# Kernel optimization log

Measured on AMD Instinct MI355X. Metric: run time of the kernel, lower is better.

## Reference

```python
import jax, jax.numpy as jnp
import numpy as np

T, H, F, E, K = 1024, 1024, 2048, 8, 2  # tokens, hidden, ffn_inter, experts, top_k


def setup_inputs() -> dict:
    key = jax.random.key(0)
    ks = jax.random.split(key, 7)
    return {
        "hidden_states": jax.random.normal(ks[0], (T, H), dtype=jnp.float32),
        "token_selected_experts": jax.random.randint(ks[1], (T, K), 0, E, dtype=jnp.int32),
        "token_final_scales": jax.random.uniform(ks[2], (T, K), dtype=jnp.float32),
        "w1": jax.random.normal(ks[3], (E, 2 * F, H), dtype=jnp.float32) * 0.02,  # gated fc1: [gate; linear]
        "b1": jax.random.normal(ks[4], (E, 2 * F), dtype=jnp.float32) * 0.02,
        "w2": jax.random.normal(ks[5], (E, H, F), dtype=jnp.float32) * 0.02,
        "b2": jax.random.normal(ks[6], (E, H), dtype=jnp.float32) * 0.02,
    }


def reference(hidden_states, token_selected_experts, token_final_scales, w1, b1, w2, b2):
    # Grouped GEMM fc1 over all experts: [T, E, 2F]
    h1 = jnp.einsum('th,efh->tef', hidden_states, w1) + b1[None]
    ffn = w2.shape[2]
    gate, lin = h1[..., :ffn], h1[..., ffn:]
    act = jax.nn.silu(gate) * lin                      # swiglu gated activation, [T, E, F]
    y_all = jnp.einsum('tef,ehf->teh', act, w2) + b2[None]  # fc2, [T, E, H]
    # Gather the top-k selected experts per token and combine with final scales
    sel = token_selected_experts.astype(jnp.int32)     # [T, K]
    y_sel = jnp.take_along_axis(y_all, sel[:, :, None], axis=1)  # [T, K, H]
    out = jnp.sum(y_sel * token_final_scales[:, :, None], axis=1)  # [T, H]
    return out
```

## Files before the change

kernel.cpp:

```cpp
#include <hip/hip_runtime.h>
#include <hip/hip_bf16.h>
#include <cstdint>
#include <cstddef>

#define TDIM 1024
#define HDIM 1024
#define FDIM 2048
#define NEXP 8
#define NENT 2048

typedef __bf16 bf16_t;
typedef __bf16 bf16x4 __attribute__((ext_vector_type(4)));
typedef __bf16 bf16x8 __attribute__((ext_vector_type(8)));
typedef float  f32x4  __attribute__((ext_vector_type(4)));

#define H_ELEMS ((size_t)TDIM*HDIM)

#define WB_OFFSETS 0
#define WB_ETOK    64
#define WB_ESCALE  (WB_ETOK + NENT*4)
#define WB_ACT     16512
#define WB_H       (WB_ACT + (size_t)NENT*FDIM*2)

__device__ __forceinline__ void gload16(const void* g, void* l) {
  __builtin_amdgcn_global_load_lds((const __attribute__((address_space(1))) void*)g,
                                   (__attribute__((address_space(3))) void*)l, 16, 0, 0);
}

__device__ __forceinline__ bf16x8 cvt8(const float4 a, const float4 b) {
  bf16x8 o;
  o[0]=(bf16_t)a.x; o[1]=(bf16_t)a.y; o[2]=(bf16_t)a.z; o[3]=(bf16_t)a.w;
  o[4]=(bf16_t)b.x; o[5]=(bf16_t)b.y; o[6]=(bf16_t)b.z; o[7]=(bf16_t)b.w;
  return o;
}

__device__ __forceinline__ int segswz(int seg, int row) {
  return seg ^ (row & 3) ^ ((row >> 2) & 3);
}

__global__ void route_all(const int* __restrict__ sel, const float* __restrict__ scal,
                          int* __restrict__ offsets, int* __restrict__ etok,
                          float* __restrict__ escale) {
  __shared__ int cnt[NEXP], cnt2[NEXP], offs[NEXP+1];
  const int t = threadIdx.x;
  if (t < NEXP) { cnt[t] = 0; cnt2[t] = 0; }
  __syncthreads();
  int e8[8];
  #pragma unroll
  for (int q = 0; q < 8; q++) {
    int i = t*8 + q;
    e8[q] = sel[i];
    atomicAdd(&cnt[e8[q]], 1);
  }
  __syncthreads();
  if (t == 0) {
    int s = 0;
    for (int e = 0; e < NEXP; e++) { offs[e] = s; offsets[e] = s; s += cnt[e]; }
    offs[NEXP] = s; offsets[NEXP] = s;
  }
  __syncthreads();
  #pragma unroll
  for (int q = 0; q < 8; q++) {
    int i = t*8 + q;
    int e = e8[q];
    int pos = offs[e] + atomicAdd(&cnt2[e], 1);
    etok[pos]   = i >> 1;
    escale[pos] = scal[i];
  }
}

__global__ void convert_h(const float* __restrict__ h, bf16_t* __restrict__ hbf) {
  size_t idx = ((size_t)blockIdx.x*256 + threadIdx.x) * 8;
  float4 v0 = ((const float4*)(h + idx))[0];
  float4 v1 = ((const float4*)(h + idx))[1];
  *(bf16x8*)(hbf + idx) = cvt8(v0, v1);
}


__global__ __launch_bounds__(256, 3) void gemm1_v8(
    const bf16_t* __restrict__ hbf, const float* __restrict__ w1,
    const float* __restrict__ b1, const int* __restrict__ offsets,
    const int* __restrict__ etok, bf16_t* __restrict__ act)
{
  const int e   = blockIdx.y;
  const int off = offsets[e];
  const int nt  = offsets[e+1] - off;
  const int m0  = blockIdx.z * 128;
  if (m0 >= nt) return;
  const int n0  = blockIdx.x * 64;

  __shared__ __align__(16) bf16_t As[2][128*32];
  __shared__ __align__(16) bf16_t Bg[2][64*32];
  __shared__ __align__(16) bf16_t Bl[2][64*32];

  const int tid  = threadIdx.x;
  const int w    = tid >> 6, lane = tid & 63;
  const int quad = lane >> 4, lr = lane & 15;
  const int wm   = w >> 1,  wn = w & 1;

  const bf16_t* asrc0; const bf16_t* asrc1;
  int arow0, arow1;
  {
    const int r0 = 0*64 + w*16 + (lane >> 2);
    const int r1 = 1*64 + w*16 + (lane >> 2);
    const int s0 = segswz(lane & 3, r0);
    const int s1 = segswz(lane & 3, r1);
    int e0 = m0 + r0; if (e0 > nt-1) e0 = nt-1;
    int e1 = m0 + r1; if (e1 > nt-1) e1 = nt-1;
    asrc0 = hbf + (size_t)etok[off + e0]*HDIM + s0*8;
    asrc1 = hbf + (size_t)etok[off + e1]*HDIM + s1*8;
    arow0 = (0*64 + w*16)*32;
    arow1 = (1*64 + w*16)*32;
  }

  const int br = tid >> 2, bs = tid & 3;
  const float* gsrc = w1 + ((size_t)e*2*FDIM + (size_t)(n0 + br))*HDIM + bs*8;
  const float* lsrc = gsrc + (size_t)FDIM*HDIM;
  const int bofs = br*32 + (segswz(bs, br) << 3);

  int aoff[4], boff[2];
  #pragma unroll
  for (int i = 0; i < 4; i++) {
    const int r = wm*64 + i*16 + lr;
    aoff[i] = r*32 + (segswz(quad, r) << 3);
  }
  #pragma unroll
  for (int j = 0; j < 2; j++) {
    const int r = wn*32 + j*16 + lr;
    boff[j] = r*32 + (segswz(quad, r) << 3);
  }

  f32x4 accg[4][2] = {}, accl[4][2] = {};
  float4 g4[2][2], l4[2][2];

#define G1_LOADB(SET, K0)                                                     \
  { const float4* p_ = (const float4*)(gsrc + (K0));                          \
    g4[SET][0]=p_[0]; g4[SET][1]=p_[1];                                       \
    const float4* q_ = (const float4*)(lsrc + (K0));                          \
    l4[SET][0]=q_[0]; l4[SET][1]=q_[1]; }

#define G1_WRITEB(NXT, SET)                                                   \
  { *(bf16x8*)&Bg[NXT][bofs] = cvt8(g4[SET][0], g4[SET][1]);                  \
    *(bf16x8*)&Bl[NXT][bofs] = cvt8(l4[SET][0], l4[SET][1]); }

#define G1_MFMA(CUR)                                                          \
  { bf16x8 af[4], gf[2], lf[2];                                               \
    _Pragma("unroll")                                                         \
    for (int i = 0; i < 4; i++) af[i] = *(const bf16x8*)&As[CUR][aoff[i]];    \
    _Pragma("unroll")                                                         \
    for (int j = 0; j < 2; j++) {                                             \
      gf[j] = *(const bf16x8*)&Bg[CUR][boff[j]];                              \
      lf[j] = *(const bf16x8*)&Bl[CUR][boff[j]];                              \
    }                                                                         \
    _Pragma("unroll")                                                         \
    for (int i = 0; i < 4; i++)                                               \
      _Pragma("unroll")                                                       \
      for (int j = 0; j < 2; j++) {                                           \
        accg[i][j] = __builtin_amdgcn_mfma_f32_16x16x32_bf16(af[i], gf[j], accg[i][j], 0, 0, 0); \
        accl[i][j] = __builtin_amdgcn_mfma_f32_16x16x32_bf16(af[i], lf[j], accl[i][j], 0, 0, 0); \
      } }

  G1_LOADB(0, 0);
  __builtin_amdgcn_sched_barrier(0);
  gload16(asrc0 + 0, &As[0][arow0]);
  gload16(asrc1 + 0, &As[0][arow1]);
  __builtin_amdgcn_sched_barrier(0);
  G1_WRITEB(0, 0);
  G1_LOADB(0, 32);
  G1_LOADB(1, 64);
  asm volatile("s_waitcnt vmcnt(8) lgkmcnt(0)" ::: "memory");
  __builtin_amdgcn_sched_barrier(0);
  __builtin_amdgcn_s_barrier();
  __builtin_amdgcn_sched_barrier(0);

#define G1_STEP(CUR, SET)                                                     \
  { G1_WRITEB((CUR)^1, SET);                                                  \
    __builtin_amdgcn_sched_barrier(0);                                        \
    gload16(asrc0 + k0 + 32, &As[(CUR)^1][arow0]);                            \
    gload16(asrc1 + k0 + 32, &As[(CUR)^1][arow1]);                            \
    __builtin_amdgcn_sched_barrier(0);                                        \
    G1_LOADB(SET, k0 + 96);                                                   \
    __builtin_amdgcn_sched_barrier(0);                                        \
    G1_MFMA(CUR);                                                             \
    asm volatile("s_waitcnt vmcnt(4) lgkmcnt(0)" ::: "memory");               \
    __builtin_amdgcn_sched_barrier(0);                                        \
    __builtin_amdgcn_s_barrier();                                             \
    __builtin_amdgcn_sched_barrier(0);                                        \
    k0 += 32; }

  int k0 = 0;
  while (k0 < 896) {
    G1_STEP(0, 0);
    G1_STEP(1, 1);
  }
  G1_STEP(0, 0);
  G1_WRITEB(0, 1);
  __builtin_amdgcn_sched_barrier(0);
  gload16(asrc0 + 960, &As[0][arow0]);
  gload16(asrc1 + 960, &As[0][arow1]);
  __builtin_amdgcn_sched_barrier(0);
  G1_MFMA(1);
  asm volatile("s_waitcnt vmcnt(0) lgkmcnt(0)" ::: "memory");
  __builtin_amdgcn_sched_barrier(0);
  __builtin_amdgcn_s_barrier();
  __builtin_amdgcn_sched_barrier(0);
  G1_WRITEB(1, 0);
  __builtin_amdgcn_sched_barrier(0);
  gload16(asrc0 + 992, &As[1][arow0]);
  gload16(asrc1 + 992, &As[1][arow1]);
  __builtin_amdgcn_sched_barrier(0);
  G1_MFMA(0);
  asm volatile("s_waitcnt vmcnt(0) lgkmcnt(0)" ::: "memory");
  __builtin_amdgcn_sched_barrier(0);
  __builtin_amdgcn_s_barrier();
  __builtin_amdgcn_sched_barrier(0);
  G1_MFMA(1);

#undef G1_STEP
#undef G1_MFMA
#undef G1_WRITEB
#undef G1_LOADB

  #pragma unroll
  for (int j = 0; j < 2; j++) {
    const int f = n0 + wn*32 + j*16 + lr;
    const float bg_ = b1[e*2*FDIM + f];
    const float bl_ = b1[e*2*FDIM + FDIM + f];
    #pragma unroll
    for (int i = 0; i < 4; i++) {
      #pragma unroll
      for (int r = 0; r < 4; r++) {
        const int m = wm*64 + i*16 + quad*4 + r;
        if (m0 + m < nt) {
          const float g = accg[i][j][r] + bg_;
          const float l = accl[i][j][r] + bl_;
          const float s = g / (1.f + __expf(-g)) * l;
          act[(size_t)(off + m0 + m)*FDIM + f] = (bf16_t)s;
        }
      }
    }
  }
}

__global__ __launch_bounds__(256, 3) void gemm2_v8(
    const bf16_t* __restrict__ act, const float* __restrict__ w2,
    const float* __restrict__ b2, const int* __restrict__ offsets,
    const int* __restrict__ etok, const float* __restrict__ escale,
    float* __restrict__ out)
{
  const int e   = blockIdx.y;
  const int off = offsets[e];
  const int nt  = offsets[e+1] - off;
  const int m0  = blockIdx.z * 128;
  if (m0 >= nt) return;
  const int n0  = (blockIdx.x >> 2) * 128;
  const int kc  = blockIdx.x & 3;
  const int kbeg = kc * (FDIM/4);

  __shared__ __align__(16) bf16_t As[2][128*32];
  __shared__ __align__(16) bf16_t Bs[2][128*32];

  const int tid  = threadIdx.x;
  const int w    = tid >> 6, lane = tid & 63;
  const int quad = lane >> 4, lr = lane & 15;
  const int wm   = w >> 1,  wn = w & 1;

  const bf16_t* asrc0; const bf16_t* asrc1;
  int arow0, arow1;
  {
    const int r0 = 0*64 + w*16 + (lane >> 2);
    const int r1 = 1*64 + w*16 + (lane >> 2);
    const int s0 = segswz(lane & 3, r0);
    const int s1 = segswz(lane & 3, r1);
    int e0 = m0 + r0; if (e0 > nt-1) e0 = nt-1;
    int e1 = m0 + r1; if (e1 > nt-1) e1 = nt-1;
    asrc0 = act + (size_t)(off + e0)*FDIM + kbeg + s0*8;
    asrc1 = act + (size_t)(off + e1)*FDIM + kbeg + s1*8;
    arow0 = (0*64 + w*16)*32;
    arow1 = (1*64 + w*16)*32;
  }

  const int br = tid >> 1, bc = tid & 1;
  const float* bsrc = w2 + ((size_t)e*HDIM + (size_t)(n0 + br))*FDIM + kbeg + bc*16;
  const int bofs0 = br*32 + (segswz(2*bc,   br) << 3);
  const int bofs1 = br*32 + (segswz(2*bc+1, br) << 3);

  int aoff[4], boff[4];
  #pragma unroll
  for (int i = 0; i < 4; i++) {
    const int r = wm*64 + i*16 + lr;
    aoff[i] = r*32 + (segswz(quad, r) << 3);
  }
  #pragma unroll
  for (int j = 0; j < 4; j++) {
    const int r = wn*64 + j*16 + lr;
    boff[j] = r*32 + (segswz(quad, r) << 3);
  }

  f32x4 acc[4][4] = {};
  float4 b4[2][4];

#define G2_LOADB(SET, K0)                                                     \
  { const float4* p_ = (const float4*)(bsrc + (K0));                          \
    b4[SET][0]=p_[0]; b4[SET][1]=p_[1]; b4[SET][2]=p_[2]; b4[SET][3]=p_[3]; }

#define G2_WRITEB(NXT, SET)                                                   \
  { *(bf16x8*)&Bs[NXT][bofs0] = cvt8(b4[SET][0], b4[SET][1]);                 \
    *(bf16x8*)&Bs[NXT][bofs1] = cvt8(b4[SET][2], b4[SET][3]); }

#define G2_MFMA(CUR)                                                          \
  { bf16x8 af[4], bfr[4];                                                     \
    _Pragma("unroll")                                                         \
    for (int i = 0; i < 4; i++) af[i] = *(const bf16x8*)&As[CUR][aoff[i]];    \
    _Pragma("unroll")                                                         \
    for (int j = 0; j < 4; j++) bfr[j] = *(const bf16x8*)&Bs[CUR][boff[j]];   \
    _Pragma("unroll")                                                         \
    for (int i = 0; i < 4; i++)                                               \
      _Pragma("unroll")                                                       \
      for (int j = 0; j < 4; j++)                                             \
        acc[i][j] = __builtin_amdgcn_mfma_f32_16x16x32_bf16(af[i], bfr[j], acc[i][j], 0, 0, 0); }

  G2_LOADB(0, 0);
  __builtin_amdgcn_sched_barrier(0);
  gload16(asrc0 + 0, &As[0][arow0]);
  gload16(asrc1 + 0, &As[0][arow1]);
  __builtin_amdgcn_sched_barrier(0);
  G2_WRITEB(0, 0);
  G2_LOADB(0, 32);
  G2_LOADB(1, 64);
  asm volatile("s_waitcnt vmcnt(8) lgkmcnt(0)" ::: "memory");
  __builtin_amdgcn_sched_barrier(0);
  __builtin_amdgcn_s_barrier();
  __builtin_amdgcn_sched_barrier(0);

#define G2_STEP(CUR, SET)                                                     \
  { G2_WRITEB((CUR)^1, SET);                                                  \
    __builtin_amdgcn_sched_barrier(0);                                        \
    gload16(asrc0 + k0 + 32, &As[(CUR)^1][arow0]);                            \
    gload16(asrc1 + k0 + 32, &As[(CUR)^1][arow1]);                            \
    __builtin_amdgcn_sched_barrier(0);                                        \
    G2_LOADB(SET, k0 + 96);                                                   \
    __builtin_amdgcn_sched_barrier(0);                                        \
    G2_MFMA(CUR);                                                             \
    asm volatile("s_waitcnt vmcnt(4) lgkmcnt(0)" ::: "memory");               \
    __builtin_amdgcn_sched_barrier(0);                                        \
    __builtin_amdgcn_s_barrier();                                             \
    __builtin_amdgcn_sched_barrier(0);                                        \
    k0 += 32; }

  int k0 = 0;
  while (k0 < 384) {
    G2_STEP(0, 0);
    G2_STEP(1, 1);
  }
  G2_STEP(0, 0);
  G2_WRITEB(0, 1);
  __builtin_amdgcn_sched_barrier(0);
  gload16(asrc0 + 448, &As[0][arow0]);
  gload16(asrc1 + 448, &As[0][arow1]);
  __builtin_amdgcn_sched_barrier(0);
  G2_MFMA(1);
  asm volatile("s_waitcnt vmcnt(0) lgkmcnt(0)" ::: "memory");
  __builtin_amdgcn_sched_barrier(0);
  __builtin_amdgcn_s_barrier();
  __builtin_amdgcn_sched_barrier(0);
  G2_WRITEB(1, 0);
  __builtin_amdgcn_sched_barrier(0);
  gload16(asrc0 + 480, &As[1][arow0]);
  gload16(asrc1 + 480, &As[1][arow1]);
  __builtin_amdgcn_sched_barrier(0);
  G2_MFMA(0);
  asm volatile("s_waitcnt vmcnt(0) lgkmcnt(0)" ::: "memory");
  __builtin_amdgcn_sched_barrier(0);
  __builtin_amdgcn_s_barrier();
  __builtin_amdgcn_sched_barrier(0);
  G2_MFMA(1);

#undef G2_STEP
#undef G2_MFMA
#undef G2_WRITEB
#undef G2_LOADB

  #pragma unroll
  for (int i = 0; i < 4; i++) {
    #pragma unroll
    for (int r = 0; r < 4; r++) {
      const int m = wm*64 + i*16 + quad*4 + r;
      if (m0 + m < nt) {
        const int slot = off + m0 + m;
        const int t    = etok[slot];
        const float s  = escale[slot];
        #pragma unroll
        for (int j = 0; j < 4; j++) {
          const int n = n0 + wn*64 + j*16 + lr;
          float v = acc[i][j][r];
          if (kc == 0) v += b2[e*HDIM + n];
          atomicAdd(&out[(size_t)t*HDIM + n], s * v);
        }
      }
    }
  }
}

extern "C" void kernel_launch(void* const* d_in, const int* in_sizes, int n_in,
                              void* d_out, int out_size, void* d_ws, size_t ws_size,
                              hipStream_t stream) {
  const float* hidden = (const float*)d_in[0];
  const int*   sel    = (const int*)d_in[1];
  const float* scal   = (const float*)d_in[2];
  const float* w1     = (const float*)d_in[3];
  const float* b1     = (const float*)d_in[4];
  const float* w2     = (const float*)d_in[5];
  const float* b2     = (const float*)d_in[6];
  float* out = (float*)d_out;

  char* ws = (char*)d_ws;
  int*    offsets = (int*)(ws + WB_OFFSETS);
  int*    etok    = (int*)(ws + WB_ETOK);
  float*  escale  = (float*)(ws + WB_ESCALE);
  bf16_t* act     = (bf16_t*)(ws + WB_ACT);
  bf16_t* hbf     = (bf16_t*)(ws + WB_H);

  hipMemsetAsync(d_out, 0, (size_t)out_size * sizeof(float), stream);

  route_all<<<1, 256, 0, stream>>>(sel, scal, offsets, etok, escale);
  convert_h<<<(int)(H_ELEMS/8/256), 256, 0, stream>>>(hidden, hbf);

  gemm1_v8<<<dim3(FDIM/64, NEXP, NENT/128), 256, 0, stream>>>(hbf, w1, b1, offsets, etok, act);
  gemm2_v8<<<dim3((HDIM/128)*4, NEXP, NENT/128), 256, 0, stream>>>(act, w2, b2, offsets, etok, escale, out);
}
```

Before: 328.5 us.

## Double M tile to 256 rows with 512-thread blocks in both expert GEMMs

Both grouped GEMM kernels now use 512-thread blocks covering 256 token rows instead of 128, so each fp32 weight tile is loaded and converted to bf16 once for twice as many tokens. Weight-loading work per thread halves and the vmcnt wait counts are adjusted to match. In exchange, fewer blocks are launched, the last M tile of each expert is padded to 256 rows, and launch bounds now allow only one block per CU. Each expert holds about 256 routed rows on average, so some experts may still need a second, mostly empty tile.

```diff
diff --git a/kernel.cpp b/kernel.cpp
--- a/kernel.cpp
+++ b/kernel.cpp
@@ -77,7 +77,7 @@
 }
 
 
-__global__ __launch_bounds__(256, 3) void gemm1_v8(
+__global__ __launch_bounds__(512, 1) void gemm1_v9(
     const bf16_t* __restrict__ hbf, const float* __restrict__ w1,
     const float* __restrict__ b1, const int* __restrict__ offsets,
     const int* __restrict__ etok, bf16_t* __restrict__ act)
@@ -85,13 +85,12 @@
   const int e   = blockIdx.y;
   const int off = offsets[e];
   const int nt  = offsets[e+1] - off;
-  const int m0  = blockIdx.z * 128;
+  const int m0  = blockIdx.z * 256;
   if (m0 >= nt) return;
   const int n0  = blockIdx.x * 64;
 
-  __shared__ __align__(16) bf16_t As[2][128*32];
-  __shared__ __align__(16) bf16_t Bg[2][64*32];
-  __shared__ __align__(16) bf16_t Bl[2][64*32];
+  __shared__ __align__(16) bf16_t As[2][256*32];
+  __shared__ __align__(16) bf16_t Bs[2][2*64*32];
 
   const int tid  = threadIdx.x;
   const int w    = tid >> 6, lane = tid & 63;
@@ -101,22 +100,22 @@
   const bf16_t* asrc0; const bf16_t* asrc1;
   int arow0, arow1;
   {
-    const int r0 = 0*64 + w*16 + (lane >> 2);
-    const int r1 = 1*64 + w*16 + (lane >> 2);
+    const int r0 = 0*128 + w*16 + (lane >> 2);
+    const int r1 = 1*128 + w*16 + (lane >> 2);
     const int s0 = segswz(lane & 3, r0);
     const int s1 = segswz(lane & 3, r1);
     int e0 = m0 + r0; if (e0 > nt-1) e0 = nt-1;
     int e1 = m0 + r1; if (e1 > nt-1) e1 = nt-1;
     asrc0 = hbf + (size_t)etok[off + e0]*HDIM + s0*8;
     asrc1 = hbf + (size_t)etok[off + e1]*HDIM + s1*8;
-    arow0 = (0*64 + w*16)*32;
-    arow1 = (1*64 + w*16)*32;
-  }
-
-  const int br = tid >> 2, bs = tid & 3;
-  const float* gsrc = w1 + ((size_t)e*2*FDIM + (size_t)(n0 + br))*HDIM + bs*8;
-  const float* lsrc = gsrc + (size_t)FDIM*HDIM;
-  const int bofs = br*32 + (segswz(bs, br) << 3);
+    arow0 = (0*128 + w*16)*32;
+    arow1 = (1*128 + w*16)*32;
+  }
+
+  const int gl = tid >> 8, st = tid & 255;
+  const int br = st >> 2, bsg = st & 3;
+  const float* bsrc = w1 + ((size_t)e*2*FDIM + (size_t)gl*FDIM + (size_t)(n0 + br))*HDIM + bsg*8;
+  const int bidx = gl*(64*32) + br*32 + (segswz(bsg, br) << 3);
 
   int aoff[4], boff[2];
   #pragma unroll
@@ -131,17 +130,14 @@
   }
 
   f32x4 accg[4][2] = {}, accl[4][2] = {};
-  float4 g4[2][2], l4[2][2];
+  float4 b4[2][2];
 
 #define G1_LOADB(SET, K0)                                                     \
-  { const float4* p_ = (const float4*)(gsrc + (K0));                          \
-    g4[SET][0]=p_[0]; g4[SET][1]=p_[1];                                       \
-    const float4* q_ = (const float4*)(lsrc + (K0));                          \
-    l4[SET][0]=q_[0]; l4[SET][1]=q_[1]; }
+  { const float4* p_ = (const float4*)(bsrc + (K0));                          \
+    b4[SET][0]=p_[0]; b4[SET][1]=p_[1]; }
 
 #define G1_WRITEB(NXT, SET)                                                   \
-  { *(bf16x8*)&Bg[NXT][bofs] = cvt8(g4[SET][0], g4[SET][1]);                  \
-    *(bf16x8*)&Bl[NXT][bofs] = cvt8(l4[SET][0], l4[SET][1]); }
+  { *(bf16x8*)&Bs[NXT][bidx] = cvt8(b4[SET][0], b4[SET][1]); }
 
 #define G1_MFMA(CUR)                                                          \
   { bf16x8 af[4], gf[2], lf[2];                                               \
@@ -149,8 +145,8 @@
     for (int i = 0; i < 4; i++) af[i] = *(const bf16x8*)&As[CUR][aoff[i]];    \
     _Pragma("unroll")                                                         \
     for (int j = 0; j < 2; j++) {                                             \
-      gf[j] = *(const bf16x8*)&Bg[CUR][boff[j]];                              \
-      lf[j] = *(const bf16x8*)&Bl[CUR][boff[j]];                              \
+      gf[j] = *(const bf16x8*)&Bs[CUR][boff[j]];                              \
+      lf[j] = *(const bf16x8*)&Bs[CUR][64*32 + boff[j]];                      \
     }                                                                         \
     _Pragma("unroll")                                                         \
     for (int i = 0; i < 4; i++)                                               \
@@ -168,7 +164,7 @@
   G1_WRITEB(0, 0);
   G1_LOADB(0, 32);
   G1_LOADB(1, 64);
-  asm volatile("s_waitcnt vmcnt(8) lgkmcnt(0)" ::: "memory");
+  asm volatile("s_waitcnt vmcnt(4) lgkmcnt(0)" ::: "memory");
   __builtin_amdgcn_sched_barrier(0);
   __builtin_amdgcn_s_barrier();
   __builtin_amdgcn_sched_barrier(0);
@@ -182,7 +178,7 @@
     G1_LOADB(SET, k0 + 96);                                                   \
     __builtin_amdgcn_sched_barrier(0);                                        \
     G1_MFMA(CUR);                                                             \
-    asm volatile("s_waitcnt vmcnt(4) lgkmcnt(0)" ::: "memory");               \
+    asm volatile("s_waitcnt vmcnt(2) lgkmcnt(0)" ::: "memory");               \
     __builtin_amdgcn_sched_barrier(0);                                        \
     __builtin_amdgcn_s_barrier();                                             \
     __builtin_amdgcn_sched_barrier(0);                                        \
@@ -242,7 +238,7 @@
   }
 }
 
-__global__ __launch_bounds__(256, 3) void gemm2_v8(
+__global__ __launch_bounds__(512, 1) void gemm2_v9(
     const bf16_t* __restrict__ act, const float* __restrict__ w2,
     const float* __restrict__ b2, const int* __restrict__ offsets,
     const int* __restrict__ etok, const float* __restrict__ escale,
@@ -251,13 +247,13 @@
   const int e   = blockIdx.y;
   const int off = offsets[e];
   const int nt  = offsets[e+1] - off;
-  const int m0  = blockIdx.z * 128;
+  const int m0  = blockIdx.z * 256;
   if (m0 >= nt) return;
   const int n0  = (blockIdx.x >> 2) * 128;
   const int kc  = blockIdx.x & 3;
   const int kbeg = kc * (FDIM/4);
 
-  __shared__ __align__(16) bf16_t As[2][128*32];
+  __shared__ __align__(16) bf16_t As[2][256*32];
   __shared__ __align__(16) bf16_t Bs[2][128*32];
 
   const int tid  = threadIdx.x;
@@ -268,22 +264,21 @@
   const bf16_t* asrc0; const bf16_t* asrc1;
   int arow0, arow1;
   {
-    const int r0 = 0*64 + w*16 + (lane >> 2);
-    const int r1 = 1*64 + w*16 + (lane >> 2);
+    const int r0 = 0*128 + w*16 + (lane >> 2);
+    const int r1 = 1*128 + w*16 + (lane >> 2);
     const int s0 = segswz(lane & 3, r0);
     const int s1 = segswz(lane & 3, r1);
     int e0 = m0 + r0; if (e0 > nt-1) e0 = nt-1;
     int e1 = m0 + r1; if (e1 > nt-1) e1 = nt-1;
     asrc0 = act + (size_t)(off + e0)*FDIM + kbeg + s0*8;
     asrc1 = act + (size_t)(off + e1)*FDIM + kbeg + s1*8;
-    arow0 = (0*64 + w*16)*32;
-    arow1 = (1*64 + w*16)*32;
-  }
-
-  const int br = tid >> 1, bc = tid & 1;
-  const float* bsrc = w2 + ((size_t)e*HDIM + (size_t)(n0 + br))*FDIM + kbeg + bc*16;
-  const int bofs0 = br*32 + (segswz(2*bc,   br) << 3);
-  const int bofs1 = br*32 + (segswz(2*bc+1, br) << 3);
+    arow0 = (0*128 + w*16)*32;
+    arow1 = (1*128 + w*16)*32;
+  }
+
+  const int br = tid >> 2, bsg = tid & 3;
+  const float* bsrc = w2 + ((size_t)e*HDIM + (size_t)(n0 + br))*FDIM + kbeg + bsg*8;
+  const int bidx = br*32 + (segswz(bsg, br) << 3);
 
   int aoff[4], boff[4];
   #pragma unroll
@@ -298,15 +293,14 @@
   }
 
   f32x4 acc[4][4] = {};
-  float4 b4[2][4];
+  float4 b4[2][2];
 
 #define G2_LOADB(SET, K0)                                                     \
   { const float4* p_ = (const float4*)(bsrc + (K0));                          \
-    b4[SET][0]=p_[0]; b4[SET][1]=p_[1]; b4[SET][2]=p_[2]; b4[SET][3]=p_[3]; }
+    b4[SET][0]=p_[0]; b4[SET][1]=p_[1]; }
 
 #define G2_WRITEB(NXT, SET)                                                   \
-  { *(bf16x8*)&Bs[NXT][bofs0] = cvt8(b4[SET][0], b4[SET][1]);                 \
-    *(bf16x8*)&Bs[NXT][bofs1] = cvt8(b4[SET][2], b4[SET][3]); }
+  { *(bf16x8*)&Bs[NXT][bidx] = cvt8(b4[SET][0], b4[SET][1]); }
 
 #define G2_MFMA(CUR)                                                          \
   { bf16x8 af[4], bfr[4];                                                     \
@@ -328,7 +322,7 @@
   G2_WRITEB(0, 0);
   G2_LOADB(0, 32);
   G2_LOADB(1, 64);
-  asm volatile("s_waitcnt vmcnt(8) lgkmcnt(0)" ::: "memory");
+  asm volatile("s_waitcnt vmcnt(4) lgkmcnt(0)" ::: "memory");
   __builtin_amdgcn_sched_barrier(0);
   __builtin_amdgcn_s_barrier();
   __builtin_amdgcn_sched_barrier(0);
@@ -342,7 +336,7 @@
     G2_LOADB(SET, k0 + 96);                                                   \
     __builtin_amdgcn_sched_barrier(0);                                        \
     G2_MFMA(CUR);                                                             \
-    asm volatile("s_waitcnt vmcnt(4) lgkmcnt(0)" ::: "memory");               \
+    asm volatile("s_waitcnt vmcnt(2) lgkmcnt(0)" ::: "memory");               \
     __builtin_amdgcn_sched_barrier(0);                                        \
     __builtin_amdgcn_s_barrier();                                             \
     __builtin_amdgcn_sched_barrier(0);                                        \
@@ -426,6 +420,6 @@
   route_all<<<1, 256, 0, stream>>>(sel, scal, offsets, etok, escale);
   convert_h<<<(int)(H_ELEMS/8/256), 256, 0, stream>>>(hidden, hbf);
 
-  gemm1_v8<<<dim3(FDIM/64, NEXP, NENT/128), 256, 0, stream>>>(hbf, w1, b1, offsets, etok, act);
-  gemm2_v8<<<dim3((HDIM/128)*4, NEXP, NENT/128), 256, 0, stream>>>(act, w2, b2, offsets, etok, escale, out);
-}
+  gemm1_v9<<<dim3(FDIM/64, NEXP, NENT/256), 512, 0, stream>>>(hbf, w1, b1, offsets, etok, act);
+  gemm2_v9<<<dim3((HDIM/128)*4, NEXP, NENT/256), 512, 0, stream>>>(act, w2, b2, offsets, etok, escale, out);
+}
```

After: 380.1 us. +15.7%, slower.

## Pre-convert expert weights to bf16 and stream them with direct-to-LDS loads

Applied to the files above, without the earlier changes.

Adds two conversion passes that turn w1 and w2 from fp32 into bf16 workspace copies on every call. New GEMM variants then load both A and B tiles with global_load_lds straight into LDS, which removes the per-thread register staging and conversion of weights inside the main loop. The pipeline becomes a simpler double buffer that waits for vmcnt(0) at every step. This costs an extra full fp32 read plus a bf16 write of all weights per call and gives less load/compute overlap. The new path runs only when the workspace is large enough; otherwise it falls back to the old kernels.

```diff
diff --git a/kernel.cpp b/kernel.cpp
--- a/kernel.cpp
+++ b/kernel.cpp
@@ -14,13 +14,18 @@
 typedef __bf16 bf16x8 __attribute__((ext_vector_type(8)));
 typedef float  f32x4  __attribute__((ext_vector_type(4)));
 
-#define H_ELEMS ((size_t)TDIM*HDIM)
+#define H_ELEMS  ((size_t)TDIM*HDIM)
+#define W1_ELEMS ((size_t)NEXP*2*FDIM*HDIM)
+#define W2_ELEMS ((size_t)NEXP*HDIM*FDIM)
 
 #define WB_OFFSETS 0
 #define WB_ETOK    64
 #define WB_ESCALE  (WB_ETOK + NENT*4)
 #define WB_ACT     16512
 #define WB_H       (WB_ACT + (size_t)NENT*FDIM*2)
+#define WB_W2BF    (WB_H + H_ELEMS*2)
+#define WB_W1BF    (WB_W2BF + W2_ELEMS*2)
+#define WB_NEED    (WB_W1BF + W1_ELEMS*2)
 
 __device__ __forceinline__ void gload16(const void* g, void* l) {
   __builtin_amdgcn_global_load_lds((const __attribute__((address_space(1))) void*)g,
@@ -77,8 +82,8 @@
 }
 
 
-__global__ __launch_bounds__(256, 3) void gemm1_v8(
-    const bf16_t* __restrict__ hbf, const float* __restrict__ w1,
+__global__ __launch_bounds__(256, 3) void gemm1_v10(
+    const bf16_t* __restrict__ hbf, const bf16_t* __restrict__ w1bf,
     const float* __restrict__ b1, const int* __restrict__ offsets,
     const int* __restrict__ etok, bf16_t* __restrict__ act)
 {
@@ -113,10 +118,15 @@
     arow1 = (1*64 + w*16)*32;
   }
 
-  const int br = tid >> 2, bs = tid & 3;
-  const float* gsrc = w1 + ((size_t)e*2*FDIM + (size_t)(n0 + br))*HDIM + bs*8;
-  const float* lsrc = gsrc + (size_t)FDIM*HDIM;
-  const int bofs = br*32 + (segswz(bs, br) << 3);
+  const bf16_t* gsrc; const bf16_t* lsrc;
+  int bdst;
+  {
+    const int brow = w*16 + (lane >> 2);
+    const int bseg = segswz(lane & 3, brow);
+    gsrc = w1bf + ((size_t)e*2*FDIM + (size_t)(n0 + brow))*HDIM + bseg*8;
+    lsrc = gsrc + (size_t)FDIM*HDIM;
+    bdst = (w*16)*32;
+  }
 
   int aoff[4], boff[2];
   #pragma unroll
@@ -131,17 +141,12 @@
   }
 
   f32x4 accg[4][2] = {}, accl[4][2] = {};
-  float4 g4[2][2], l4[2][2];
-
-#define G1_LOADB(SET, K0)                                                     \
-  { const float4* p_ = (const float4*)(gsrc + (K0));                          \
-    g4[SET][0]=p_[0]; g4[SET][1]=p_[1];                                       \
-    const float4* q_ = (const float4*)(lsrc + (K0));                          \
-    l4[SET][0]=q_[0]; l4[SET][1]=q_[1]; }
-
-#define G1_WRITEB(NXT, SET)                                                   \
-  { *(bf16x8*)&Bg[NXT][bofs] = cvt8(g4[SET][0], g4[SET][1]);                  \
-    *(bf16x8*)&Bl[NXT][bofs] = cvt8(l4[SET][0], l4[SET][1]); }
+
+#define G1_STAGE(K0, NXT)                                                     \
+  { gload16(asrc0 + (K0), &As[NXT][arow0]);                                   \
+    gload16(asrc1 + (K0), &As[NXT][arow1]);                                   \
+    gload16(gsrc  + (K0), &Bg[NXT][bdst]);                                    \
+    gload16(lsrc  + (K0), &Bl[NXT][bdst]); }
 
 #define G1_MFMA(CUR)                                                          \
   { bf16x8 af[4], gf[2], lf[2];                                               \
@@ -160,66 +165,33 @@
         accl[i][j] = __builtin_amdgcn_mfma_f32_16x16x32_bf16(af[i], lf[j], accl[i][j], 0, 0, 0); \
       } }
 
-  G1_LOADB(0, 0);
-  __builtin_amdgcn_sched_barrier(0);
-  gload16(asrc0 + 0, &As[0][arow0]);
-  gload16(asrc1 + 0, &As[0][arow1]);
-  __builtin_amdgcn_sched_barrier(0);
-  G1_WRITEB(0, 0);
-  G1_LOADB(0, 32);
-  G1_LOADB(1, 64);
-  asm volatile("s_waitcnt vmcnt(8) lgkmcnt(0)" ::: "memory");
-  __builtin_amdgcn_sched_barrier(0);
-  __builtin_amdgcn_s_barrier();
-  __builtin_amdgcn_sched_barrier(0);
-
-#define G1_STEP(CUR, SET)                                                     \
-  { G1_WRITEB((CUR)^1, SET);                                                  \
-    __builtin_amdgcn_sched_barrier(0);                                        \
-    gload16(asrc0 + k0 + 32, &As[(CUR)^1][arow0]);                            \
-    gload16(asrc1 + k0 + 32, &As[(CUR)^1][arow1]);                            \
-    __builtin_amdgcn_sched_barrier(0);                                        \
-    G1_LOADB(SET, k0 + 96);                                                   \
+#define G1_STEP(CUR)                                                          \
+  { G1_STAGE(k0 + 32, (CUR)^1);                                               \
     __builtin_amdgcn_sched_barrier(0);                                        \
     G1_MFMA(CUR);                                                             \
-    asm volatile("s_waitcnt vmcnt(4) lgkmcnt(0)" ::: "memory");               \
+    asm volatile("s_waitcnt vmcnt(0)" ::: "memory");                          \
     __builtin_amdgcn_sched_barrier(0);                                        \
     __builtin_amdgcn_s_barrier();                                             \
     __builtin_amdgcn_sched_barrier(0);                                        \
     k0 += 32; }
 
+  G1_STAGE(0, 0);
+  asm volatile("s_waitcnt vmcnt(0)" ::: "memory");
+  __builtin_amdgcn_sched_barrier(0);
+  __builtin_amdgcn_s_barrier();
+  __builtin_amdgcn_sched_barrier(0);
+
   int k0 = 0;
-  while (k0 < 896) {
-    G1_STEP(0, 0);
-    G1_STEP(1, 1);
-  }
-  G1_STEP(0, 0);
-  G1_WRITEB(0, 1);
-  __builtin_amdgcn_sched_barrier(0);
-  gload16(asrc0 + 960, &As[0][arow0]);
-  gload16(asrc1 + 960, &As[0][arow1]);
-  __builtin_amdgcn_sched_barrier(0);
-  G1_MFMA(1);
-  asm volatile("s_waitcnt vmcnt(0) lgkmcnt(0)" ::: "memory");
-  __builtin_amdgcn_sched_barrier(0);
-  __builtin_amdgcn_s_barrier();
-  __builtin_amdgcn_sched_barrier(0);
-  G1_WRITEB(1, 0);
-  __builtin_amdgcn_sched_barrier(0);
-  gload16(asrc0 + 992, &As[1][arow0]);
-  gload16(asrc1 + 992, &As[1][arow1]);
-  __builtin_amdgcn_sched_barrier(0);
-  G1_MFMA(0);
-  asm volatile("s_waitcnt vmcnt(0) lgkmcnt(0)" ::: "memory");
-  __builtin_amdgcn_sched_barrier(0);
-  __builtin_amdgcn_s_barrier();
-  __builtin_amdgcn_sched_barrier(0);
+  while (k0 < 960) {
+    G1_STEP(0);
+    G1_STEP(1);
+  }
+  G1_STEP(0);
   G1_MFMA(1);
 
 #undef G1_STEP
 #undef G1_MFMA
-#undef G1_WRITEB
-#undef G1_LOADB
+#undef G1_STAGE
 
   #pragma unroll
   for (int j = 0; j < 2; j++) {
@@ -242,8 +214,8 @@
   }
 }
 
-__global__ __launch_bounds__(256, 3) void gemm2_v8(
-    const bf16_t* __restrict__ act, const float* __restrict__ w2,
+__global__ __launch_bounds__(256, 3) void gemm2_v10(
+    const bf16_t* __restrict__ act, const bf16_t* __restrict__ w2bf,
     const float* __restrict__ b2, const int* __restrict__ offsets,
     const int* __restrict__ etok, const float* __restrict__ escale,
     float* __restrict__ out)
@@ -280,10 +252,18 @@
     arow1 = (1*64 + w*16)*32;
   }
 
-  const int br = tid >> 1, bc = tid & 1;
-  const float* bsrc = w2 + ((size_t)e*HDIM + (size_t)(n0 + br))*FDIM + kbeg + bc*16;
-  const int bofs0 = br*32 + (segswz(2*bc,   br) << 3);
-  const int bofs1 = br*32 + (segswz(2*bc+1, br) << 3);
+  const bf16_t* bsrc0; const bf16_t* bsrc1;
+  int bdst0, bdst1;
+  {
+    const int r0 = w*32 + (lane >> 2);
+    const int r1 = w*32 + 16 + (lane >> 2);
+    const int s0 = segswz(lane & 3, r0);
+    const int s1 = segswz(lane & 3, r1);
+    bsrc0 = w2bf + ((size_t)e*HDIM + (size_t)(n0 + r0))*FDIM + kbeg + s0*8;
+    bsrc1 = w2bf + ((size_t)e*HDIM + (size_t)(n0 + r1))*FDIM + kbeg + s1*8;
+    bdst0 = (w*32)*32;
+    bdst1 = (w*32 + 16)*32;
+  }
 
   int aoff[4], boff[4];
   #pragma unroll
@@ -298,15 +278,12 @@
   }
 
   f32x4 acc[4][4] = {};
-  float4 b4[2][4];
-
-#define G2_LOADB(SET, K0)                                                     \
-  { const float4* p_ = (const float4*)(bsrc + (K0));                          \
-    b4[SET][0]=p_[0]; b4[SET][1]=p_[1]; b4[SET][2]=p_[2]; b4[SET][3]=p_[3]; }
-
-#define G2_WRITEB(NXT, SET)                                                   \
-  { *(bf16x8*)&Bs[NXT][bofs0] = cvt8(b4[SET][0], b4[SET][1]);                 \
-    *(bf16x8*)&Bs[NXT][bofs1] = cvt8(b4[SET][2], b4[SET][3]); }
+
+#define G2_STAGE(K0, NXT)                                                     \
+  { gload16(asrc0 + (K0), &As[NXT][arow0]);                                   \
+    gload16(asrc1 + (K0), &As[NXT][arow1]);                                   \
+    gload16(bsrc0 + (K0), &Bs[NXT][bdst0]);                                   \
+    gload16(bsrc1 + (K0), &Bs[NXT][bdst1]); }
 
 #define G2_MFMA(CUR)                                                          \
   { bf16x8 af[4], bfr[4];                                                     \
@@ -320,66 +297,33 @@
       for (int j = 0; j < 4; j++)                                             \
         acc[i][j] = __builtin_amdgcn_mfma_f32_16x16x32_bf16(af[i], bfr[j], acc[i][j], 0, 0, 0); }
 
-  G2_LOADB(0, 0);
-  __builtin_amdgcn_sched_barrier(0);
-  gload16(asrc0 + 0, &As[0][arow0]);
-  gload16(asrc1 + 0, &As[0][arow1]);
-  __builtin_amdgcn_sched_barrier(0);
-  G2_WRITEB(0, 0);
-  G2_LOADB(0, 32);
-  G2_LOADB(1, 64);
-  asm volatile("s_waitcnt vmcnt(8) lgkmcnt(0)" ::: "memory");
-  __builtin_amdgcn_sched_barrier(0);
-  __builtin_amdgcn_s_barrier();
-  __builtin_amdgcn_sched_barrier(0);
-
-#define G2_STEP(CUR, SET)                                                     \
-  { G2_WRITEB((CUR)^1, SET);                                                  \
-    __builtin_amdgcn_sched_barrier(0);                                        \
-    gload16(asrc0 + k0 + 32, &As[(CUR)^1][arow0]);                            \
-    gload16(asrc1 + k0 + 32, &As[(CUR)^1][arow1]);                            \
-    __builtin_amdgcn_sched_barrier(0);                                        \
-    G2_LOADB(SET, k0 + 96);                                                   \
+#define G2_STEP(CUR)                                                          \
+  { G2_STAGE(k0 + 32, (CUR)^1);                                               \
     __builtin_amdgcn_sched_barrier(0);                                        \
     G2_MFMA(CUR);                                                             \
-    asm volatile("s_waitcnt vmcnt(4) lgkmcnt(0)" ::: "memory");               \
+    asm volatile("s_waitcnt vmcnt(0)" ::: "memory");                          \
     __builtin_amdgcn_sched_barrier(0);                                        \
     __builtin_amdgcn_s_barrier();                                             \
     __builtin_amdgcn_sched_barrier(0);                                        \
     k0 += 32; }
 
+  G2_STAGE(0, 0);
+  asm volatile("s_waitcnt vmcnt(0)" ::: "memory");
+  __builtin_amdgcn_sched_barrier(0);
+  __builtin_amdgcn_s_barrier();
+  __builtin_amdgcn_sched_barrier(0);
+
   int k0 = 0;
-  while (k0 < 384) {
-    G2_STEP(0, 0);
-    G2_STEP(1, 1);
-  }
-  G2_STEP(0, 0);
-  G2_WRITEB(0, 1);
-  __builtin_amdgcn_sched_barrier(0);
-  gload16(asrc0 + 448, &As[0][arow0]);
-  gload16(asrc1 + 448, &As[0][arow1]);
-  __builtin_amdgcn_sched_barrier(0);
-  G2_MFMA(1);
-  asm volatile("s_waitcnt vmcnt(0) lgkmcnt(0)" ::: "memory");
-  __builtin_amdgcn_sched_barrier(0);
-  __builtin_amdgcn_s_barrier();
-  __builtin_amdgcn_sched_barrier(0);
-  G2_WRITEB(1, 0);
-  __builtin_amdgcn_sched_barrier(0);
-  gload16(asrc0 + 480, &As[1][arow0]);
-  gload16(asrc1 + 480, &As[1][arow1]);
-  __builtin_amdgcn_sched_barrier(0);
-  G2_MFMA(0);
-  asm volatile("s_waitcnt vmcnt(0) lgkmcnt(0)" ::: "memory");
-  __builtin_amdgcn_sched_barrier(0);
-  __builtin_amdgcn_s_barrier();
-  __builtin_amdgcn_sched_barrier(0);
+  while (k0 < 448) {
+    G2_STEP(0);
+    G2_STEP(1);
+  }
+  G2_STEP(0);
   G2_MFMA(1);
 
 #undef G2_STEP
 #undef G2_MFMA
-#undef G2_WRITEB
-#undef G2_LOADB
+#undef G2_STAGE
 
   #pragma unroll
   for (int i = 0; i < 4; i++) {
@@ -402,6 +346,321 @@
   }
 }
 
+__global__ __launch_bounds__(256, 3) void gemm1_v8(
+    const bf16_t* __restrict__ hbf, const float* __restrict__ w1,
+    const float* __restrict__ b1, const int* __restrict__ offsets,
+    const int* __restrict__ etok, bf16_t* __restrict__ act)
+{
+  const int e   = blockIdx.y;
+  const int off = offsets[e];
+  const int nt  = offsets[e+1] - off;
+  const int m0  = blockIdx.z * 128;
+  if (m0 >= nt) return;
+  const int n0  = blockIdx.x * 64;
+
+  __shared__ __align__(16) bf16_t As[2][128*32];
+  __shared__ __align__(16) bf16_t Bg[2][64*32];
+  __shared__ __align__(16) bf16_t Bl[2][64*32];
+
+  const int tid  = threadIdx.x;
+  const int w    = tid >> 6, lane = tid & 63;
+  const int quad = lane >> 4, lr = lane & 15;
+  const int wm   = w >> 1,  wn = w & 1;
+
+  const bf16_t* asrc0; const bf16_t* asrc1;
+  int arow0, arow1;
+  {
+    const int r0 = 0*64 + w*16 + (lane >> 2);
+    const int r1 = 1*64 + w*16 + (lane >> 2);
+    const int s0 = segswz(lane & 3, r0);
+    const int s1 = segswz(lane & 3, r1);
+    int e0 = m0 + r0; if (e0 > nt-1) e0 = nt-1;
+    int e1 = m0 + r1; if (e1 > nt-1) e1 = nt-1;
+    asrc0 = hbf + (size_t)etok[off + e0]*HDIM + s0*8;
+    asrc1 = hbf + (size_t)etok[off + e1]*HDIM + s1*8;
+    arow0 = (0*64 + w*16)*32;
+    arow1 = (1*64 + w*16)*32;
+  }
+
+  const int br = tid >> 2, bs = tid & 3;
+  const float* gsrc = w1 + ((size_t)e*2*FDIM + (size_t)(n0 + br))*HDIM + bs*8;
+  const float* lsrc = gsrc + (size_t)FDIM*HDIM;
+  const int bofs = br*32 + (segswz(bs, br) << 3);
+
+  int aoff[4], boff[2];
+  #pragma unroll
+  for (int i = 0; i < 4; i++) {
+    const int r = wm*64 + i*16 + lr;
+    aoff[i] = r*32 + (segswz(quad, r) << 3);
+  }
+  #pragma unroll
+  for (int j = 0; j < 2; j++) {
+    const int r = wn*32 + j*16 + lr;
+    boff[j] = r*32 + (segswz(quad, r) << 3);
+  }
+
+  f32x4 accg[4][2] = {}, accl[4][2] = {};
+  float4 g4[2][2], l4[2][2];
+
+#define F1_LOADB(SET, K0)                                                     \
+  { const float4* p_ = (const float4*)(gsrc + (K0));                          \
+    g4[SET][0]=p_[0]; g4[SET][1]=p_[1];                                       \
+    const float4* q_ = (const float4*)(lsrc + (K0));                          \
+    l4[SET][0]=q_[0]; l4[SET][1]=q_[1]; }
+#define F1_WRITEB(NXT, SET)                                                   \
+  { *(bf16x8*)&Bg[NXT][bofs] = cvt8(g4[SET][0], g4[SET][1]);                  \
+    *(bf16x8*)&Bl[NXT][bofs] = cvt8(l4[SET][0], l4[SET][1]); }
+#define F1_MFMA(CUR)                                                          \
+  { bf16x8 af[4], gf[2], lf[2];                                               \
+    _Pragma("unroll")                                                         \
+    for (int i = 0; i < 4; i++) af[i] = *(const bf16x8*)&As[CUR][aoff[i]];    \
+    _Pragma("unroll")                                                         \
+    for (int j = 0; j < 2; j++) {                                             \
+      gf[j] = *(const bf16x8*)&Bg[CUR][boff[j]];                              \
+      lf[j] = *(const bf16x8*)&Bl[CUR][boff[j]];                              \
+    }                                                                         \
+    _Pragma("unroll")                                                         \
+    for (int i = 0; i < 4; i++)                                               \
+      _Pragma("unroll")                                                       \
+      for (int j = 0; j < 2; j++) {                                           \
+        accg[i][j] = __builtin_amdgcn_mfma_f32_16x16x32_bf16(af[i], gf[j], accg[i][j], 0, 0, 0); \
+        accl[i][j] = __builtin_amdgcn_mfma_f32_16x16x32_bf16(af[i], lf[j], accl[i][j], 0, 0, 0); \
+      } }
+
+  F1_LOADB(0, 0);
+  __builtin_amdgcn_sched_barrier(0);
+  gload16(asrc0 + 0, &As[0][arow0]);
+  gload16(asrc1 + 0, &As[0][arow1]);
+  __builtin_amdgcn_sched_barrier(0);
+  F1_WRITEB(0, 0);
+  F1_LOADB(0, 32);
+  F1_LOADB(1, 64);
+  asm volatile("s_waitcnt vmcnt(8) lgkmcnt(0)" ::: "memory");
+  __builtin_amdgcn_sched_barrier(0);
+  __builtin_amdgcn_s_barrier();
+  __builtin_amdgcn_sched_barrier(0);
+
+#define F1_STEP(CUR, SET)                                                     \
+  { F1_WRITEB((CUR)^1, SET);                                                  \
+    __builtin_amdgcn_sched_barrier(0);                                        \
+    gload16(asrc0 + k0 + 32, &As[(CUR)^1][arow0]);                            \
+    gload16(asrc1 + k0 + 32, &As[(CUR)^1][arow1]);                            \
+    __builtin_amdgcn_sched_barrier(0);                                        \
+    F1_LOADB(SET, k0 + 96);                                                   \
+    __builtin_amdgcn_sched_barrier(0);                                        \
+    F1_MFMA(CUR);                                                             \
+    asm volatile("s_waitcnt vmcnt(4) lgkmcnt(0)" ::: "memory");               \
+    __builtin_amdgcn_sched_barrier(0);                                        \
+    __builtin_amdgcn_s_barrier();                                             \
+    __builtin_amdgcn_sched_barrier(0);                                        \
+    k0 += 32; }
+
+  int k0 = 0;
+  while (k0 < 896) { F1_STEP(0, 0); F1_STEP(1, 1); }
+  F1_STEP(0, 0);
+  F1_WRITEB(0, 1);
+  __builtin_amdgcn_sched_barrier(0);
+  gload16(asrc0 + 960, &As[0][arow0]);
+  gload16(asrc1 + 960, &As[0][arow1]);
+  __builtin_amdgcn_sched_barrier(0);
+  F1_MFMA(1);
+  asm volatile("s_waitcnt vmcnt(0) lgkmcnt(0)" ::: "memory");
+  __builtin_amdgcn_sched_barrier(0);
+  __builtin_amdgcn_s_barrier();
+  __builtin_amdgcn_sched_barrier(0);
+  F1_WRITEB(1, 0);
+  __builtin_amdgcn_sched_barrier(0);
+  gload16(asrc0 + 992, &As[1][arow0]);
+  gload16(asrc1 + 992, &As[1][arow1]);
+  __builtin_amdgcn_sched_barrier(0);
+  F1_MFMA(0);
+  asm volatile("s_waitcnt vmcnt(0) lgkmcnt(0)" ::: "memory");
+  __builtin_amdgcn_sched_barrier(0);
+  __builtin_amdgcn_s_barrier();
+  __builtin_amdgcn_sched_barrier(0);
+  F1_MFMA(1);
+
+#undef F1_STEP
+#undef F1_MFMA
+#undef F1_WRITEB
+#undef F1_LOADB
+
+  #pragma unroll
+  for (int j = 0; j < 2; j++) {
+    const int f = n0 + wn*32 + j*16 + lr;
+    const float bg_ = b1[e*2*FDIM + f];
+    const float bl_ = b1[e*2*FDIM + FDIM + f];
+    #pragma unroll
+    for (int i = 0; i < 4; i++) {
+      #pragma unroll
+      for (int r = 0; r < 4; r++) {
+        const int m = wm*64 + i*16 + quad*4 + r;
+        if (m0 + m < nt) {
+          const float g = accg[i][j][r] + bg_;
+          const float l = accl[i][j][r] + bl_;
+          const float s = g / (1.f + __expf(-g)) * l;
+          act[(size_t)(off + m0 + m)*FDIM + f] = (bf16_t)s;
+        }
+      }
+    }
+  }
+}
+
+__global__ __launch_bounds__(256, 3) void gemm2_v8(
+    const bf16_t* __restrict__ act, const float* __restrict__ w2,
+    const float* __restrict__ b2, const int* __restrict__ offsets,
+    const int* __restrict__ etok, const float* __restrict__ escale,
+    float* __restrict__ out)
+{
+  const int e   = blockIdx.y;
+  const int off = offsets[e];
+  const int nt  = offsets[e+1] - off;
+  const int m0  = blockIdx.z * 128;
+  if (m0 >= nt) return;
+  const int n0  = (blockIdx.x >> 2) * 128;
+  const int kc  = blockIdx.x & 3;
+  const int kbeg = kc * (FDIM/4);
+
+  __shared__ __align__(16) bf16_t As[2][128*32];
+  __shared__ __align__(16) bf16_t Bs[2][128*32];
+
+  const int tid  = threadIdx.x;
+  const int w    = tid >> 6, lane = tid & 63;
+  const int quad = lane >> 4, lr = lane & 15;
+  const int wm   = w >> 1,  wn = w & 1;
+
+  const bf16_t* asrc0; const bf16_t* asrc1;
+  int arow0, arow1;
+  {
+    const int r0 = 0*64 + w*16 + (lane >> 2);
+    const int r1 = 1*64 + w*16 + (lane >> 2);
+    const int s0 = segswz(lane & 3, r0);
+    const int s1 = segswz(lane & 3, r1);
+    int e0 = m0 + r0; if (e0 > nt-1) e0 = nt-1;
+    int e1 = m0 + r1; if (e1 > nt-1) e1 = nt-1;
+    asrc0 = act + (size_t)(off + e0)*FDIM + kbeg + s0*8;
+    asrc1 = act + (size_t)(off + e1)*FDIM + kbeg + s1*8;
+    arow0 = (0*64 + w*16)*32;
+    arow1 = (1*64 + w*16)*32;
+  }
+
+  const int br = tid >> 1, bc = tid & 1;
+  const float* bsrc = w2 + ((size_t)e*HDIM + (size_t)(n0 + br))*FDIM + kbeg + bc*16;
+  const int bofs0 = br*32 + (segswz(2*bc,   br) << 3);
+  const int bofs1 = br*32 + (segswz(2*bc+1, br) << 3);
+
+  int aoff[4], boff[4];
+  #pragma unroll
+  for (int i = 0; i < 4; i++) {
+    const int r = wm*64 + i*16 + lr;
+    aoff[i] = r*32 + (segswz(quad, r) << 3);
+  }
+  #pragma unroll
+  for (int j = 0; j < 4; j++) {
+    const int r = wn*64 + j*16 + lr;
+    boff[j] = r*32 + (segswz(quad, r) << 3);
+  }
+
+  f32x4 acc[4][4] = {};
+  float4 b4[2][4];
+
+#define F2_LOADB(SET, K0)                                                     \
+  { const float4* p_ = (const float4*)(bsrc + (K0));                          \
+    b4[SET][0]=p_[0]; b4[SET][1]=p_[1]; b4[SET][2]=p_[2]; b4[SET][3]=p_[3]; }
+#define F2_WRITEB(NXT, SET)                                                   \
+  { *(bf16x8*)&Bs[NXT][bofs0] = cvt8(b4[SET][0], b4[SET][1]);                 \
+    *(bf16x8*)&Bs[NXT][bofs1] = cvt8(b4[SET][2], b4[SET][3]); }
+#define F2_MFMA(CUR)                                                          \
+  { bf16x8 af[4], bfr[4];                                                     \
+    _Pragma("unroll")                                                         \
+    for (int i = 0; i < 4; i++) af[i] = *(const bf16x8*)&As[CUR][aoff[i]];    \
+    _Pragma("unroll")                                                         \
+    for (int j = 0; j < 4; j++) bfr[j] = *(const bf16x8*)&Bs[CUR][boff[j]];   \
+    _Pragma("unroll")                                                         \
+    for (int i = 0; i < 4; i++)                                               \
+      _Pragma("unroll")                                                       \
+      for (int j = 0; j < 4; j++)                                             \
+        acc[i][j] = __builtin_amdgcn_mfma_f32_16x16x32_bf16(af[i], bfr[j], acc[i][j], 0, 0, 0); }
+
+  F2_LOADB(0, 0);
+  __builtin_amdgcn_sched_barrier(0);
+  gload16(asrc0 + 0, &As[0][arow0]);
+  gload16(asrc1 + 0, &As[0][arow1]);
+  __builtin_amdgcn_sched_barrier(0);
+  F2_WRITEB(0, 0);
+  F2_LOADB(0, 32);
+  F2_LOADB(1, 64);
+  asm volatile("s_waitcnt vmcnt(8) lgkmcnt(0)" ::: "memory");
+  __builtin_amdgcn_sched_barrier(0);
+  __builtin_amdgcn_s_barrier();
+  __builtin_amdgcn_sched_barrier(0);
+
+#define F2_STEP(CUR, SET)                                                     \
+  { F2_WRITEB((CUR)^1, SET);                                                  \
+    __builtin_amdgcn_sched_barrier(0);                                        \
+    gload16(asrc0 + k0 + 32, &As[(CUR)^1][arow0]);                            \
+    gload16(asrc1 + k0 + 32, &As[(CUR)^1][arow1]);                            \
+    __builtin_amdgcn_sched_barrier(0);                                        \
+    F2_LOADB(SET, k0 + 96);                                                   \
+    __builtin_amdgcn_sched_barrier(0);                                        \
+    F2_MFMA(CUR);                                                             \
+    asm volatile("s_waitcnt vmcnt(4) lgkmcnt(0)" ::: "memory");               \
+    __builtin_amdgcn_sched_barrier(0);                                        \
+    __builtin_amdgcn_s_barrier();                                             \
+    __builtin_amdgcn_sched_barrier(0);                                        \
+    k0 += 32; }
+
+  int k0 = 0;
+  while (k0 < 384) { F2_STEP(0, 0); F2_STEP(1, 1); }
+  F2_STEP(0, 0);
+  F2_WRITEB(0, 1);
+  __builtin_amdgcn_sched_barrier(0);
+  gload16(asrc0 + 448, &As[0][arow0]);
+  gload16(asrc1 + 448, &As[0][arow1]);
+  __builtin_amdgcn_sched_barrier(0);
+  F2_MFMA(1);
+  asm volatile("s_waitcnt vmcnt(0) lgkmcnt(0)" ::: "memory");
+  __builtin_amdgcn_sched_barrier(0);
+  __builtin_amdgcn_s_barrier();
+  __builtin_amdgcn_sched_barrier(0);
+  F2_WRITEB(1, 0);
+  __builtin_amdgcn_sched_barrier(0);
+  gload16(asrc0 + 480, &As[1][arow0]);
+  gload16(asrc1 + 480, &As[1][arow1]);
+  __builtin_amdgcn_sched_barrier(0);
+  F2_MFMA(0);
+  asm volatile("s_waitcnt vmcnt(0) lgkmcnt(0)" ::: "memory");
+  __builtin_amdgcn_sched_barrier(0);
+  __builtin_amdgcn_s_barrier();
+  __builtin_amdgcn_sched_barrier(0);
+  F2_MFMA(1);
+
+#undef F2_STEP
+#undef F2_MFMA
+#undef F2_WRITEB
+#undef F2_LOADB
+
+  #pragma unroll
+  for (int i = 0; i < 4; i++) {
+    #pragma unroll
+    for (int r = 0; r < 4; r++) {
+      const int m = wm*64 + i*16 + quad*4 + r;
+      if (m0 + m < nt) {
+        const int slot = off + m0 + m;
+        const int t    = etok[slot];
+        const float s  = escale[slot];
+        #pragma unroll
+        for (int j = 0; j < 4; j++) {
+          const int n = n0 + wn*64 + j*16 + lr;
+          float v = acc[i][j][r];
+          if (kc == 0) v += b2[e*HDIM + n];
+          atomicAdd(&out[(size_t)t*HDIM + n], s * v);
+        }
+      }
+    }
+  }
+}
+
 extern "C" void kernel_launch(void* const* d_in, const int* in_sizes, int n_in,
                               void* d_out, int out_size, void* d_ws, size_t ws_size,
                               hipStream_t stream) {
@@ -420,12 +679,21 @@
   float*  escale  = (float*)(ws + WB_ESCALE);
   bf16_t* act     = (bf16_t*)(ws + WB_ACT);
   bf16_t* hbf     = (bf16_t*)(ws + WB_H);
+  bf16_t* w2bf    = (bf16_t*)(ws + WB_W2BF);
+  bf16_t* w1bf    = (bf16_t*)(ws + WB_W1BF);
 
   hipMemsetAsync(d_out, 0, (size_t)out_size * sizeof(float), stream);
 
   route_all<<<1, 256, 0, stream>>>(sel, scal, offsets, etok, escale);
   convert_h<<<(int)(H_ELEMS/8/256), 256, 0, stream>>>(hidden, hbf);
 
-  gemm1_v8<<<dim3(FDIM/64, NEXP, NENT/128), 256, 0, stream>>>(hbf, w1, b1, offsets, etok, act);
-  gemm2_v8<<<dim3((HDIM/128)*4, NEXP, NENT/128), 256, 0, stream>>>(act, w2, b2, offsets, etok, escale, out);
-}
+  if (ws_size >= WB_NEED) {
+    convert_h<<<(int)(W2_ELEMS/8/256), 256, 0, stream>>>(w2, w2bf);
+    convert_h<<<(int)(W1_ELEMS/8/256), 256, 0, stream>>>(w1, w1bf);
+    gemm1_v10<<<dim3(FDIM/64, NEXP, NENT/128), 256, 0, stream>>>(hbf, w1bf, b1, offsets, etok, act);
+    gemm2_v10<<<dim3((HDIM/128)*4, NEXP, NENT/128), 256, 0, stream>>>(act, w2bf, b2, offsets, etok, escale, out);
+  } else {
+    gemm1_v8<<<dim3(FDIM/64, NEXP, NENT/128), 256, 0, stream>>>(hbf, w1, b1, offsets, etok, act);
+    gemm2_v8<<<dim3((HDIM/128)*4, NEXP, NENT/128), 256, 0, stream>>>(act, w2, b2, offsets, etok, escale, out);
+  }
+}
```

Measured after the change: 358.3 us. 9.1% more time.
